# Kernel optimization log

Hardware: AMD Instinct MI355X
Metric: run time of the kernel (lower is better)

Reference implementation:

```python
import jax, jax.numpy as jnp
import numpy as np

LENGTH = 320  # hard-coded in the layer
BIG = 1e5     # cap for 'no zero pixel in column' distances; BIG**2 = 1e10 -> exp() underflows to 0


def _edt_sq(zero):
    """Exact squared Euclidean distance transform.

    zero: [N, H, W] bool, True where the uint8-restored mask is 0 (seed pixels).
    Returns [N, H, W] float32 squared distance of every pixel to the nearest seed.
    Phase 1: 1D distance along H via associative scans (nearest seed above/below).
    Phase 2: exact lower envelope over W via a vectorized min-reduction:
             D2[n,i,j] = min_x ( (j-x)^2 + g2[n,i,x] ).
    """
    N, H, W = zero.shape
    ih = jnp.arange(H, dtype=jnp.float32)[None, :, None]            # [1,H,1]
    last = jax.lax.associative_scan(jnp.maximum,
                                    jnp.where(zero, ih, -BIG), axis=1)
    nxt = jax.lax.associative_scan(jnp.minimum,
                                   jnp.where(zero, ih, 2.0 * BIG), axis=1,
                                   reverse=True)
    g = jnp.minimum(jnp.minimum(ih - last, nxt - ih), BIG)           # [N,H,W] 1D dist
    g2 = g * g
    jw = jnp.arange(W, dtype=jnp.float32)
    off = (jw[:, None] - jw[None, :]) ** 2                           # [Wj, Wx]
    # [N,H,Wj,Wx] broadcast + min over source column x
    d2 = jnp.min(g2[:, :, None, :] + off[None, None], axis=-1)
    return d2


def _forward(inputs):
    B, H, W, _ = inputs.shape
    # uint8 cast: zero iff (1-x)*127.5 < 1  (matches tf.cast truncation)
    restored = ((1.0 - jax.lax.stop_gradient(inputs)) * 127.5).astype(jnp.uint8)
    zero = restored == 0                                             # [B,H,W,2]
    zm = jnp.moveaxis(zero, -1, 1).reshape(B * 2, H, W)              # fold channel into batch
    d2 = _edt_sq(zm).reshape(B, 2, H, W)
    sigmas = jnp.asarray([0.02, 0.08, 0.16], jnp.float32) * LENGTH   # [3]
    denom = 2.0 * sigmas * sigmas
    # exp(-d^2 / (2 sigma^2)) for each (channel, sigma); channel-major order like the loop
    clicks = jnp.exp(-d2[:, :, None] / denom[None, None, :, None, None])  # [B,2,3,H,W]
    return jnp.moveaxis(clicks.reshape(B, 6, H, W), 1, -1)          # [B,H,W,6]


def setup_inputs() -> dict:
    key = jax.random.key(0)
    inputs = jax.random.uniform(key, (4, 320, 320, 2), dtype=jnp.float32)
    return {"inputs": inputs}


def reference(inputs):
    return _forward(inputs)
```

## Files before the change

### kernel.cpp

```cpp
#include <hip/hip_runtime.h>

#define HH 320
#define WW 320
#define NIMG 8
#define BIGF 1.0e5f

#define TW  16
#define NCH 32
#define CH  10

__global__ __launch_bounds__(512) void edt_vert(const float* __restrict__ in,
                                                float* __restrict__ g2) {
    int wl = threadIdx.x;
    int ch = threadIdx.y;
    int b  = blockIdx.x / 20;
    int wt = blockIdx.x % 20;
    int w  = wt * TW + wl;
    int h0 = ch * CH;

    const float2* ip = (const float2*)in + (size_t)(b * HH + h0) * WW + w;
    float2 v[CH];
    #pragma unroll
    for (int k = 0; k < CH; ++k) v[k] = ip[(size_t)k * WW];

    unsigned m0 = 0, m1 = 0;
    #pragma unroll
    for (int k = 0; k < CH; ++k) {
        if ((1.0f - v[k].x) * 127.5f < 1.0f) m0 |= 1u << k;
        if ((1.0f - v[k].y) * 127.5f < 1.0f) m1 |= 1u << k;
    }

    __shared__ float sL[2][NCH][TW], sN[2][NCH][TW];
    sL[0][ch][wl] = m0 ? (float)(h0 + 31 - __clz((int)m0)) : -1.0e9f;
    sL[1][ch][wl] = m1 ? (float)(h0 + 31 - __clz((int)m1)) : -1.0e9f;
    sN[0][ch][wl] = m0 ? (float)(h0 + __ffs((int)m0) - 1)  :  1.0e9f;
    sN[1][ch][wl] = m1 ? (float)(h0 + __ffs((int)m1) - 1)  :  1.0e9f;
    __syncthreads();

    float L0 = -1.0e9f, L1 = -1.0e9f, N0 = 1.0e9f, N1 = 1.0e9f;
    for (int cc = 0; cc < NCH; ++cc) {
        float a0 = sL[0][cc][wl], a1 = sL[1][cc][wl];
        float b0 = sN[0][cc][wl], b1 = sN[1][cc][wl];
        if (cc < ch) { L0 = fmaxf(L0, a0); L1 = fmaxf(L1, a1); }
        if (cc > ch) { N0 = fminf(N0, b0); N1 = fminf(N1, b1); }
    }

    float gd0[CH], gd1[CH];
    float r0 = L0, r1 = L1;
    #pragma unroll
    for (int k = 0; k < CH; ++k) {
        float fh = (float)(h0 + k);
        if (m0 & (1u << k)) r0 = fh;
        if (m1 & (1u << k)) r1 = fh;
        gd0[k] = fh - r0;
        gd1[k] = fh - r1;
    }
    float* gp0 = g2 + ((size_t)(b * 2 + 0) * HH + h0) * WW + w;
    float* gp1 = g2 + ((size_t)(b * 2 + 1) * HH + h0) * WW + w;
    r0 = N0; r1 = N1;
    #pragma unroll
    for (int k = CH - 1; k >= 0; --k) {
        float fh = (float)(h0 + k);
        if (m0 & (1u << k)) r0 = fh;
        if (m1 & (1u << k)) r1 = fh;
        float g0 = fminf(fminf(gd0[k], r0 - fh), BIGF);
        float g1 = fminf(fminf(gd1[k], r1 - fh), BIGF);
        gp0[(size_t)k * WW] = g0 * g0;
        gp1[(size_t)k * WW] = g1 * g1;
    }
}

__global__ __launch_bounds__(256) void edt_horiz(const float* __restrict__ g2,
                                                 float* __restrict__ out) {
    int wv   = threadIdx.x >> 6;
    int lane = threadIdx.x & 63;
    int row  = blockIdx.x * 4 + wv;
    int n = row / HH;
    int h = row - n * HH;
    int b = n >> 1, c = n & 1;

    __shared__ __align__(16) float sa[4][WW + 8];
    const float* grow = g2 + (size_t)row * WW;
    #pragma unroll
    for (int m = 0; m < 5; ++m) {
        int x = lane + 64 * m;
        float fx = (float)x;
        sa[wv][x] = fmaf(fx, fx, grow[x]);
    }
    if (lane < 8) sa[wv][WW + lane] = 3.0e38f;

    float n2j[5], d2v[5];
    #pragma unroll
    for (int m = 0; m < 5; ++m) {
        n2j[m] = -2.0f * (float)(lane + 64 * m);
        d2v[m] = 3.4e38f;
    }

    const float4* sv = (const float4*)sa[wv];
    float4 c0 = sv[0], c1 = sv[1];
    for (int xc = 0; xc < WW / 4; xc += 2) {
        float4 p0 = sv[xc + 2], p1 = sv[xc + 3];
        float av[8] = {c0.x, c0.y, c0.z, c0.w, c1.x, c1.y, c1.z, c1.w};
        float base = (float)(4 * xc);
        #pragma unroll
        for (int k = 0; k < 8; k += 2) {
            float x0 = base + (float)k;
            float x1 = base + (float)(k + 1);
            #pragma unroll
            for (int m = 0; m < 5; ++m) {
                float t0 = fmaf(n2j[m], x0, av[k]);
                float t1 = fmaf(n2j[m], x1, av[k + 1]);
                d2v[m] = fminf(d2v[m], fminf(t0, t1));
            }
        }
        c0 = p0; c1 = p1;
    }

    float* op = out + (((size_t)b * HH + h) * WW + lane) * 6 + (size_t)c * 3;
    #pragma unroll
    for (int m = 0; m < 5; ++m) {
        float fj = (float)(lane + 64 * m);
        float d2 = fmaf(fj, fj, d2v[m]);
        float* q = op + (size_t)m * 64 * 6;
        q[0] = __expf(-d2 * (1.0f / 81.92f));
        q[1] = __expf(-d2 * (1.0f / 1310.72f));
        q[2] = __expf(-d2 * (1.0f / 5242.88f));
    }
}

extern "C" void kernel_launch(void* const* d_in, const int* in_sizes, int n_in,
                              void* d_out, int out_size, void* d_ws, size_t ws_size,
                              hipStream_t stream) {
    const float* in = (const float*)d_in[0];
    float* out = (float*)d_out;
    float* g2 = (float*)d_ws;

    edt_vert<<<4 * 20, dim3(TW, NCH), 0, stream>>>(in, g2);
    edt_horiz<<<NIMG * HH / 4, 256, 0, stream>>>(g2, out);
}
```

Measured before the change: 75.15 us.

## Prune horizontal EDT scan with chunk lower bounds and coalesce output stores

The horizontal pass now scans each lane's local 32-column chunks first, then expands outward chunk by chunk. A chunk is skipped when a wave-wide lower bound built from the squared column gap plus the chunk's minimum g2 cannot beat the current best. Blocks are regrouped so each block handles both channels for two rows. Results are staged in shared memory and written as coalesced float4 stores of all six outputs, replacing the strided scalar stores. This adds divergent control flow and wave votes, and the amount of work saved depends on the data.

```diff
diff --git a/kernel.cpp b/kernel.cpp
--- a/kernel.cpp
+++ b/kernel.cpp
@@ -74,57 +74,117 @@
                                                  float* __restrict__ out) {
     int wv   = threadIdx.x >> 6;
     int lane = threadIdx.x & 63;
-    int row  = blockIdx.x * 4 + wv;
-    int n = row / HH;
-    int h = row - n * HH;
-    int b = n >> 1, c = n & 1;
-
-    __shared__ __align__(16) float sa[4][WW + 8];
+    int b  = blockIdx.x / 160;
+    int hp = blockIdx.x % 160;
+    int hh = wv >> 1;
+    int c  = wv & 1;
+    int row = (2 * b + c) * HH + (2 * hp + hh);
+
+    __shared__ __align__(16) float sa[4][WW];
+    __shared__ float scm[4][10];
+    __shared__ float sd2[2][2][WW];
+
     const float* grow = g2 + (size_t)row * WW;
     #pragma unroll
     for (int m = 0; m < 5; ++m) {
         int x = lane + 64 * m;
+        float g = grow[x];
         float fx = (float)x;
-        sa[wv][x] = fmaf(fx, fx, grow[x]);
-    }
-    if (lane < 8) sa[wv][WW + lane] = 3.0e38f;
-
-    float n2j[5], d2v[5];
-    #pragma unroll
-    for (int m = 0; m < 5; ++m) {
+        sa[wv][x] = fmaf(fx, fx, g);
+        float v = g;
+        v = fminf(v, __shfl_xor(v, 1));
+        v = fminf(v, __shfl_xor(v, 2));
+        v = fminf(v, __shfl_xor(v, 4));
+        v = fminf(v, __shfl_xor(v, 8));
+        v = fminf(v, __shfl_xor(v, 16));
+        if ((lane & 31) == 0) scm[wv][2 * m + (lane >> 5)] = v;
+    }
+
+    const float4* sv = (const float4*)sa[wv];
+    float d2v[5], n2j[5];
+    #pragma unroll
+    for (int m = 0; m < 5; ++m) {
+        d2v[m] = 3.4e38f;
         n2j[m] = -2.0f * (float)(lane + 64 * m);
-        d2v[m] = 3.4e38f;
-    }
-
-    const float4* sv = (const float4*)sa[wv];
-    float4 c0 = sv[0], c1 = sv[1];
-    for (int xc = 0; xc < WW / 4; xc += 2) {
-        float4 p0 = sv[xc + 2], p1 = sv[xc + 3];
-        float av[8] = {c0.x, c0.y, c0.z, c0.w, c1.x, c1.y, c1.z, c1.w};
-        float base = (float)(4 * xc);
+    }
+
+    auto scanChunk = [&](int m, int ck) {
+        int q0 = ck * 8;
         #pragma unroll
-        for (int k = 0; k < 8; k += 2) {
-            float x0 = base + (float)k;
-            float x1 = base + (float)(k + 1);
+        for (int u = 0; u < 8; u += 2) {
+            float4 f0 = sv[q0 + u];
+            float4 f1 = sv[q0 + u + 1];
+            float xb = (float)(ck * 32 + 4 * u);
+            float av[8] = {f0.x, f0.y, f0.z, f0.w, f1.x, f1.y, f1.z, f1.w};
             #pragma unroll
-            for (int m = 0; m < 5; ++m) {
-                float t0 = fmaf(n2j[m], x0, av[k]);
-                float t1 = fmaf(n2j[m], x1, av[k + 1]);
+            for (int k = 0; k < 8; k += 2) {
+                float t0 = fmaf(n2j[m], xb + (float)k,       av[k]);
+                float t1 = fmaf(n2j[m], xb + (float)(k + 1), av[k + 1]);
                 d2v[m] = fminf(d2v[m], fminf(t0, t1));
             }
         }
-        c0 = p0; c1 = p1;
-    }
-
-    float* op = out + (((size_t)b * HH + h) * WW + lane) * 6 + (size_t)c * 3;
+    };
+
+    #pragma unroll
+    for (int m = 0; m < 5; ++m) { scanChunk(m, 2 * m); scanChunk(m, 2 * m + 1); }
+
+    for (int m = 0; m < 5; ++m) {
+        float fj  = (float)(lane + 64 * m);
+        float fj2 = fj * fj;
+        bool goL = (m > 0), goR = (m < 4);
+        for (int r = 1; r < 10 && (goL || goR); ++r) {
+            int cl = 2 * m - r, cr = 2 * m + 1 + r;
+            if (goL) {
+                if (cl < 0) goL = false;
+                else {
+                    float thr = d2v[m] + fj2;
+                    float gap = fj - (float)(32 * cl + 31);
+                    float bb = gap * gap;
+                    if (!__any(bb < thr)) goL = false;
+                    else if (__any(bb + scm[wv][cl] < thr)) scanChunk(m, cl);
+                }
+            }
+            if (goR) {
+                if (cr > 9) goR = false;
+                else {
+                    float thr = d2v[m] + fj2;
+                    float gap = (float)(32 * cr) - fj;
+                    float bb = gap * gap;
+                    if (!__any(bb < thr)) goR = false;
+                    else if (__any(bb + scm[wv][cr] < thr)) scanChunk(m, cr);
+                }
+            }
+        }
+    }
+
     #pragma unroll
     for (int m = 0; m < 5; ++m) {
         float fj = (float)(lane + 64 * m);
-        float d2 = fmaf(fj, fj, d2v[m]);
-        float* q = op + (size_t)m * 64 * 6;
-        q[0] = __expf(-d2 * (1.0f / 81.92f));
-        q[1] = __expf(-d2 * (1.0f / 1310.72f));
-        q[2] = __expf(-d2 * (1.0f / 5242.88f));
+        sd2[hh][c][lane + 64 * m] = fmaf(fj, fj, d2v[m]);
+    }
+    __syncthreads();
+
+    float* obase = out + (size_t)(b * HH + 2 * hp) * WW * 6;
+    for (int q = threadIdx.x; q < 960; q += 256) {
+        int D = 4 * q;
+        int hh2 = D / 1920;
+        int rr = D - 1920 * hh2;
+        float vals[4];
+        #pragma unroll
+        for (int e = 0; e < 4; ++e) {
+            int idx = rr + e;
+            int jj = idx / 6;
+            int cs = idx - 6 * jj;
+            int c2 = (cs >= 3) ? 1 : 0;
+            int s  = cs - 3 * c2;
+            float dd = sd2[hh2][c2][jj];
+            float co = (s == 0) ? (1.0f / 81.92f)
+                     : (s == 1) ? (1.0f / 1310.72f)
+                                : (1.0f / 5242.88f);
+            vals[e] = __expf(-dd * co);
+        }
+        float4 o = {vals[0], vals[1], vals[2], vals[3]};
+        *(float4*)(obase + D) = o;
     }
 }
 
@@ -136,5 +196,5 @@
     float* g2 = (float*)d_ws;
 
     edt_vert<<<4 * 20, dim3(TW, NCH), 0, stream>>>(in, g2);
-    edt_horiz<<<NIMG * HH / 4, 256, 0, stream>>>(g2, out);
+    edt_horiz<<<4 * 160, 256, 0, stream>>>(g2, out);
 }
```

Measured after the change: 86.28 us. +14.8%, slower.
